# Performance work log

Hardware: AMD Instinct MI355X
Metric: run time of the kernel (lower is better)

## Reference

```python
import jax, jax.numpy as jnp
import numpy as np

N, E, H = 100000, 3200000, 128


def setup_inputs() -> dict:
    key = jax.random.key(0)
    ks = jax.random.split(key, 12)
    s = 1.0 / np.sqrt(H)
    x = jax.random.normal(ks[0], (N, H), dtype=jnp.float32)
    edge_index = jax.random.randint(ks[1], (2, E), 0, N, dtype=jnp.int64)
    # GatedGraphConv weight: [num_layers=1, H, H] -> single [H, H]
    W = jax.random.normal(ks[2], (H, H), dtype=jnp.float32) * s
    # GRUCell (gate order: r, z, n)
    gru_w_ih = jax.random.normal(ks[3], (3 * H, H), dtype=jnp.float32) * s
    gru_w_hh = jax.random.normal(ks[4], (3 * H, H), dtype=jnp.float32) * s
    gru_b_ih = jax.random.normal(ks[5], (3 * H,), dtype=jnp.float32) * s
    gru_b_hh = jax.random.normal(ks[6], (3 * H,), dtype=jnp.float32) * s
    # LSTM layer 0 (gate order: i, f, g, o)
    lstm_w_ih = jax.random.normal(ks[7], (4 * H, H), dtype=jnp.float32) * s
    lstm_w_hh = jax.random.normal(ks[8], (4 * H, H), dtype=jnp.float32) * s
    lstm_b_ih = jax.random.normal(ks[9], (4 * H,), dtype=jnp.float32) * s
    lstm_b_hh = jax.random.normal(ks[10], (4 * H,), dtype=jnp.float32) * s
    return {
        "x": x, "edge_index": edge_index, "W": W,
        "gru_w_ih": gru_w_ih, "gru_w_hh": gru_w_hh,
        "gru_b_ih": gru_b_ih, "gru_b_hh": gru_b_hh,
        "lstm_w_ih": lstm_w_ih, "lstm_w_hh": lstm_w_hh,
        "lstm_b_ih": lstm_b_ih, "lstm_b_hh": lstm_b_hh,
    }


def _forward(x, edge_index, W, gru_w_ih, gru_w_hh, gru_b_ih, gru_b_hh,
             lstm_w_ih, lstm_w_hh, lstm_b_ih, lstm_b_hh):
    n = x.shape[0]
    src, dst = edge_index[0], edge_index[1]
    # GatedGraphConv, num_layers=1, mean aggregation
    m = x @ W                                   # [N, H]
    msg = m[src]                                # [E, H] gather (memory-bound)
    agg_sum = jax.ops.segment_sum(msg, dst, num_segments=n)
    deg = jax.ops.segment_sum(jnp.ones((src.shape[0],), x.dtype), dst, num_segments=n)
    agg = agg_sum / jnp.maximum(deg, 1.0)[:, None]
    # GRUCell(agg, x): gates r, z, n
    gi = agg @ gru_w_ih.T + gru_b_ih
    gh = x @ gru_w_hh.T + gru_b_hh
    i_r, i_z, i_n = jnp.split(gi, 3, axis=-1)
    h_r, h_z, h_n = jnp.split(gh, 3, axis=-1)
    r = jax.nn.sigmoid(i_r + h_r)
    z = jax.nn.sigmoid(i_z + h_z)
    ng = jnp.tanh(i_n + r * h_n)
    h_conv = (1.0 - z) * ng + z * x             # conv output H_tilde
    # 1-layer LSTM over seq_len=1 with zero initial (H, C)
    gates = h_conv @ lstm_w_ih.T + lstm_b_ih + lstm_b_hh  # h0 = 0
    i_g, f_g, g_g, o_g = jnp.split(gates, 4, axis=-1)
    c = jax.nn.sigmoid(i_g) * jnp.tanh(g_g)
    h_lstm = jax.nn.sigmoid(o_g) * jnp.tanh(c)
    return jax.nn.relu(h_lstm)


def reference(x, edge_index, W, gru_w_ih, gru_w_hh, gru_b_ih, gru_b_hh,
              lstm_w_ih, lstm_w_hh, lstm_b_ih, lstm_b_hh):
    return _forward(x, edge_index, W, gru_w_ih, gru_w_hh, gru_b_ih, gru_b_hh,
                    lstm_w_ih, lstm_w_hh, lstm_b_ih, lstm_b_hh)
```

## Files before the change

### kernel.cpp

```cpp
#include <hip/hip_runtime.h>
#include <math.h>

#define HD 128
#define PB 256
#define SCB 4096

typedef __attribute__((ext_vector_type(8))) short short8;
typedef __attribute__((ext_vector_type(4))) float f32x4;

__device__ __forceinline__ float sigf(float v) { return 1.0f / (1.0f + __expf(-v)); }

__device__ __forceinline__ unsigned short f2bf(float f) {
  union { float f; unsigned u; } v; v.f = f;
  unsigned r = (v.u + 0x7fffu + ((v.u >> 16) & 1u)) >> 16;
  return (unsigned short)r;
}
__device__ __forceinline__ float bf2f(unsigned short b) {
  union { unsigned u; float f; } v; v.u = ((unsigned)b) << 16;
  return v.f;
}


__global__ __launch_bounds__(256) void bcount_k(const int* __restrict__ ei,
                                                int* __restrict__ bcnt,
                                                int E, int N, int shift, int NB) {
  __shared__ int h[256];
  const int blk = blockIdx.x, tid = threadIdx.x;
  h[tid] = 0;
  __syncthreads();
  int per = (E + PB - 1) / PB;
  int lo = blk * per;
  int hi = (lo + per < E) ? lo + per : E;
  for (int e = lo + tid; e < hi; e += 256) {
    int d = ei[(size_t)E + e];
    if ((unsigned)d >= (unsigned)N) continue;
    atomicAdd(&h[d >> shift], 1);
  }
  __syncthreads();
  if (tid < NB) bcnt[tid * PB + blk] = h[tid];
}

__global__ __launch_bounds__(256) void scan1_k(const int* __restrict__ a,
                                               int* __restrict__ bsums, int total) {
  __shared__ int ts[256];
  int b = blockIdx.x, tid = threadIdx.x;
  int lo = b * SCB + tid * 16;
  int s = 0;
#pragma unroll
  for (int i = 0; i < 16; ++i) {
    int idx = lo + i;
    if (idx < total) s += a[idx];
  }
  ts[tid] = s;
  __syncthreads();
  for (int off = 128; off > 0; off >>= 1) {
    if (tid < off) ts[tid] += ts[tid + off];
    __syncthreads();
  }
  if (tid == 0) bsums[b] = ts[0];
}

__global__ __launch_bounds__(256) void scan2_k(int* __restrict__ bsums, int nb) {
  __shared__ int ts[256];
  int tid = threadIdx.x;
  int v = (tid < nb) ? bsums[tid] : 0;
  ts[tid] = v;
  __syncthreads();
  for (int off = 1; off < 256; off <<= 1) {
    int u = (tid >= off) ? ts[tid - off] : 0;
    __syncthreads();
    ts[tid] += u;
    __syncthreads();
  }
  if (tid < nb) bsums[tid] = ts[tid] - v;
}

__global__ __launch_bounds__(256) void scan3_k(int* __restrict__ a,
                                               const int* __restrict__ bsums,
                                               int total, int nblk) {
  __shared__ int ts[256];
  int b = blockIdx.x, tid = threadIdx.x;
  int lo = b * SCB + tid * 16;
  int pre[16];
  int s = 0;
#pragma unroll
  for (int i = 0; i < 16; ++i) {
    int idx = lo + i;
    int xv = (idx < total) ? a[idx] : 0;
    pre[i] = s;
    s += xv;
  }
  ts[tid] = s;
  __syncthreads();
  for (int off = 1; off < 256; off <<= 1) {
    int u = (tid >= off) ? ts[tid - off] : 0;
    __syncthreads();
    ts[tid] += u;
    __syncthreads();
  }
  int off0 = ts[tid] - s + bsums[b];
#pragma unroll
  for (int i = 0; i < 16; ++i) {
    int idx = lo + i;
    if (idx < total) a[idx] = off0 + pre[i];
  }
  if (b == nblk - 1 && tid == 255) a[total] = off0 + s;
}

__global__ __launch_bounds__(256) void bpart_k(const int* __restrict__ ei,
                                               const int* __restrict__ bstart,
                                               int2* __restrict__ ebuf,
                                               int E, int N, int shift, int NB) {
  __shared__ int cur[256];
  const int blk = blockIdx.x, tid = threadIdx.x;
  if (tid < NB) cur[tid] = bstart[tid * PB + blk];
  __syncthreads();
  int per = (E + PB - 1) / PB;
  int lo = blk * per;
  int hi = (lo + per < E) ? lo + per : E;
  for (int e = lo + tid; e < hi; e += 256) {
    int s = ei[e];
    int d = ei[(size_t)E + e];
    if ((unsigned)s >= (unsigned)N || (unsigned)d >= (unsigned)N) continue;
    int p = atomicAdd(&cur[d >> shift], 1);
    ebuf[p] = make_int2(s, d);
  }
}

__global__ __launch_bounds__(256) void bfill2_k(const int2* __restrict__ ebuf,
                                                const int* __restrict__ bstart,
                                                int* __restrict__ rowstart,
                                                int* __restrict__ csr,
                                                int N, int shift, int NB) {
  __shared__ int cnt[2048];
  __shared__ int tsum[256];
  const int b = blockIdx.x, tid = threadIdx.x;
  const int d0 = b << shift;
  int dmax = d0 + (1 << shift);
  if (dmax > N) dmax = N;
  const int nd = dmax - d0;
  for (int i = tid; i < nd; i += 256) cnt[i] = 0;
  __syncthreads();
  const int base = bstart[b * PB];
  const int end = bstart[(b + 1) * PB];
  for (int idx = base + tid; idx < end; idx += 256)
    atomicAdd(&cnt[ebuf[idx].y - d0], 1);
  __syncthreads();
  const int C = (nd + 255) / 256;
  int lo = tid * C;
  int hi = (lo + C < nd) ? lo + C : nd;
  int loc[8];
  int s = 0;
  for (int i = lo; i < hi; ++i) {
    loc[i - lo] = cnt[i];
    s += cnt[i];
  }
  tsum[tid] = s;
  __syncthreads();
  for (int off = 1; off < 256; off <<= 1) {
    int u = (tid >= off) ? tsum[tid - off] : 0;
    __syncthreads();
    tsum[tid] += u;
    __syncthreads();
  }
  int run = tsum[tid] - s + base;
  for (int i = lo; i < hi; ++i) {
    rowstart[d0 + i] = run;
    cnt[i] = run;
    run += loc[i - lo];
  }
  if (b == NB - 1 && tid == 255) rowstart[N] = end;
  __syncthreads();
  for (int idx = base + tid; idx < end; idx += 256) {
    int2 sd = ebuf[idx];
    int p = atomicAdd(&cnt[sd.y - d0], 1);
    csr[p] = sd.x;
  }
}


__global__ __launch_bounds__(256) void convx_k(const float* __restrict__ x,
                                               unsigned short* __restrict__ xb, int n4) {
  int t = blockIdx.x * 256 + threadIdx.x;
  if (t >= n4) return;
  float4 v = reinterpret_cast<const float4*>(x)[t];
  ushort4 o;
  o.x = f2bf(v.x); o.y = f2bf(v.y); o.z = f2bf(v.z); o.w = f2bf(v.w);
  reinterpret_cast<ushort4*>(xb)[t] = o;
}

__global__ __launch_bounds__(256) void prepw_k(
    const float* __restrict__ W, const float* __restrict__ gwih,
    const float* __restrict__ gwhh, const float* __restrict__ lwih,
    const float* __restrict__ lbih, const float* __restrict__ lbhh,
    unsigned short* __restrict__ Wt, unsigned short* __restrict__ gwihb,
    unsigned short* __restrict__ gwhhb, unsigned short* __restrict__ lwb,
    float* __restrict__ lbias) {
  int t = blockIdx.x * 256 + threadIdx.x;
  if (t < 16384) {
    int n = t >> 7, k = t & 127;
    Wt[t] = f2bf(W[(size_t)k * 128 + n]);
    return;
  }
  t -= 16384;
  if (t < 49152) { gwihb[t] = f2bf(gwih[t]); return; }
  t -= 49152;
  if (t < 49152) { gwhhb[t] = f2bf(gwhh[t]); return; }
  t -= 49152;
  if (t < 49152) {
    int j = t >> 7, k = t & 127;
    int jm = j < 128 ? j : j + 128;
    lwb[t] = f2bf(lwih[(size_t)jm * 128 + k]);
    return;
  }
  t -= 49152;
  if (t < 384) {
    int jm = t < 128 ? t : t + 128;
    lbias[t] = lbih[jm] + lbhh[jm];
  }
}


__global__ __launch_bounds__(256) void gather_b_k(const int* __restrict__ csr,
                                                  const int* __restrict__ rowstart,
                                                  const unsigned short* __restrict__ xb,
                                                  unsigned short* __restrict__ xaggb, int N) {
  int w = (int)(((long long)blockIdx.x * 256 + threadIdx.x) >> 6);
  if (w >= N) return;
  int lane = threadIdx.x & 63;
  int beg = rowstart[w], end = rowstart[w + 1];
  const unsigned* x1 = reinterpret_cast<const unsigned*>(xb);
  float ax = 0.f, ay = 0.f;
  int j = beg;
  for (; j + 4 <= end; j += 4) {
    int s0 = csr[j], s1 = csr[j + 1], s2 = csr[j + 2], s3 = csr[j + 3];
    unsigned u0 = x1[(size_t)s0 * 64 + lane];
    unsigned u1 = x1[(size_t)s1 * 64 + lane];
    unsigned u2 = x1[(size_t)s2 * 64 + lane];
    unsigned u3 = x1[(size_t)s3 * 64 + lane];
    ax += bf2f((unsigned short)u0) + bf2f((unsigned short)u1) +
          bf2f((unsigned short)u2) + bf2f((unsigned short)u3);
    ay += bf2f((unsigned short)(u0 >> 16)) + bf2f((unsigned short)(u1 >> 16)) +
          bf2f((unsigned short)(u2 >> 16)) + bf2f((unsigned short)(u3 >> 16));
  }
  for (; j < end; ++j) {
    unsigned u = x1[(size_t)csr[j] * 64 + lane];
    ax += bf2f((unsigned short)u);
    ay += bf2f((unsigned short)(u >> 16));
  }
  float scale = 1.0f / fmaxf((float)(end - beg), 1.0f);
  unsigned o = (unsigned)f2bf(ax * scale) | ((unsigned)f2bf(ay * scale) << 16);
  reinterpret_cast<unsigned*>(xaggb)[(size_t)w * 64 + lane] = o;
}

__global__ __launch_bounds__(256) void gemmw_k(const unsigned short* __restrict__ A,
                                               const unsigned short* __restrict__ B,
                                               unsigned short* __restrict__ C, int nrows) {
  __shared__ unsigned short Bs[64][136];
  const int tid = threadIdx.x;
  const int w = tid >> 6, lane = tid & 63;
  const int q = lane >> 4, r = lane & 15;
  const int row0 = blockIdx.y * 64;
  const int col0 = blockIdx.x * 64;

#pragma unroll
  for (int i = 0; i < 4; ++i) {
    int idx = i * 256 + tid;
    int c = idx >> 4, kq = idx & 15;
    uint4 v = *reinterpret_cast<const uint4*>(&B[((size_t)(col0 + c)) * HD + kq * 8]);
    *reinterpret_cast<uint4*>(&Bs[c][kq * 8]) = v;
  }
  __syncthreads();

  int arow = row0 + (w << 4) + r;
  int ar = arow < nrows ? arow : nrows - 1;
  const unsigned short* Ap = A + (size_t)ar * HD + q * 8;

  f32x4 acc[4];
#pragma unroll
  for (int cb = 0; cb < 4; ++cb) acc[cb] = (f32x4)0.f;

#pragma unroll
  for (int ks = 0; ks < 4; ++ks) {
    short8 af = *reinterpret_cast<const short8*>(Ap + ks * 32);
#pragma unroll
    for (int cb = 0; cb < 4; ++cb) {
      short8 bf = *reinterpret_cast<const short8*>(&Bs[cb * 16 + r][ks * 32 + q * 8]);
      acc[cb] = __builtin_amdgcn_mfma_f32_16x16x32_bf16(af, bf, acc[cb], 0, 0, 0);
    }
  }

#pragma unroll
  for (int cb = 0; cb < 4; ++cb) {
    int col = col0 + cb * 16 + r;
#pragma unroll
    for (int reg = 0; reg < 4; ++reg) {
      int row = row0 + (w << 4) + q * 4 + reg;
      if (row < nrows) C[(size_t)row * HD + col] = f2bf(acc[cb][reg]);
    }
  }
}

__global__ __launch_bounds__(256) void gru_fused_k(
    const unsigned short* __restrict__ Acb, const unsigned short* __restrict__ xb,
    const unsigned short* __restrict__ gwihb, const unsigned short* __restrict__ gwhhb,
    const float* __restrict__ gbih, const float* __restrict__ gbhh,
    unsigned short* __restrict__ hconv, int nrows) {
  __shared__ unsigned short Bsm[6][32][136];
  const int tid = threadIdx.x;
  const int w = tid >> 6, lane = tid & 63;
  const int q = lane >> 4, r = lane & 15;
  const int row0 = blockIdx.y * 64;
  const int c0 = blockIdx.x * 32;

#pragma unroll
  for (int it = 0; it < 12; ++it) {
    int idx = it * 256 + tid;
    int p = idx >> 9;
    int rem = idx & 511;
    int col = rem >> 4, kq = rem & 15;
    const unsigned short* src =
        (p < 3) ? gwihb + ((size_t)(p * 128 + c0 + col)) * HD
                : gwhhb + ((size_t)((p - 3) * 128 + c0 + col)) * HD;
    uint4 v = *reinterpret_cast<const uint4*>(src + kq * 8);
    *reinterpret_cast<uint4*>(&Bsm[p][col][kq * 8]) = v;
  }
  __syncthreads();

  int arow = row0 + (w << 4) + r;
  int ar = arow < nrows ? arow : nrows - 1;
  const unsigned short* Aa = Acb + (size_t)ar * HD + q * 8;
  const unsigned short* Ax = xb + (size_t)ar * HD + q * 8;

  f32x4 acc[6][2];
#pragma unroll
  for (int p = 0; p < 6; ++p)
#pragma unroll
    for (int cb = 0; cb < 2; ++cb) acc[p][cb] = (f32x4)0.f;

#pragma unroll
  for (int ks = 0; ks < 4; ++ks) {
    short8 a1 = *reinterpret_cast<const short8*>(Aa + ks * 32);
    short8 a2 = *reinterpret_cast<const short8*>(Ax + ks * 32);
#pragma unroll
    for (int p = 0; p < 6; ++p) {
      short8 af = (p < 3) ? a1 : a2;
#pragma unroll
      for (int cb = 0; cb < 2; ++cb) {
        short8 bf = *reinterpret_cast<const short8*>(&Bsm[p][cb * 16 + r][ks * 32 + q * 8]);
        acc[p][cb] = __builtin_amdgcn_mfma_f32_16x16x32_bf16(af, bf, acc[p][cb], 0, 0, 0);
      }
    }
  }

#pragma unroll
  for (int cb = 0; cb < 2; ++cb) {
    int col = c0 + cb * 16 + r;
    float bir = gbih[col], biz = gbih[col + 128], bin = gbih[col + 256];
    float bhr = gbhh[col], bhz = gbhh[col + 128], bhn = gbhh[col + 256];
#pragma unroll
    for (int reg = 0; reg < 4; ++reg) {
      int row = row0 + (w << 4) + q * 4 + reg;
      if (row < nrows) {
        float ir = acc[0][cb][reg] + bir, iz = acc[1][cb][reg] + biz;
        float inn = acc[2][cb][reg] + bin;
        float hr = acc[3][cb][reg] + bhr, hz = acc[4][cb][reg] + bhz;
        float hn = acc[5][cb][reg] + bhn;
        float rr = sigf(ir + hr), zz = sigf(iz + hz);
        float nn = tanhf(inn + rr * hn);
        float xv = bf2f(xb[(size_t)row * HD + col]);
        hconv[(size_t)row * HD + col] = f2bf((1.f - zz) * nn + zz * xv);
      }
    }
  }
}

__global__ __launch_bounds__(256) void lstm_fused_k(
    const unsigned short* __restrict__ hconv, const unsigned short* __restrict__ lwb,
    const float* __restrict__ lbias, float* __restrict__ out, int nrows) {
  __shared__ unsigned short Bsm[3][64][136];
  const int tid = threadIdx.x;
  const int w = tid >> 6, lane = tid & 63;
  const int q = lane >> 4, r = lane & 15;
  const int row0 = blockIdx.y * 64;
  const int c0 = blockIdx.x * 64;

#pragma unroll
  for (int it = 0; it < 12; ++it) {
    int idx = it * 256 + tid;
    int p = idx >> 10, rem = idx & 1023;
    int col = rem >> 4, kq = rem & 15;
    uint4 v = *reinterpret_cast<const uint4*>(
        lwb + ((size_t)(p * 128 + c0 + col)) * HD + kq * 8);
    *reinterpret_cast<uint4*>(&Bsm[p][col][kq * 8]) = v;
  }
  __syncthreads();

  int arow = row0 + (w << 4) + r;
  int ar = arow < nrows ? arow : nrows - 1;
  const unsigned short* Ap = hconv + (size_t)ar * HD + q * 8;

  f32x4 acc[3][4];
#pragma unroll
  for (int p = 0; p < 3; ++p)
#pragma unroll
    for (int cb = 0; cb < 4; ++cb) acc[p][cb] = (f32x4)0.f;

#pragma unroll
  for (int ks = 0; ks < 4; ++ks) {
    short8 af = *reinterpret_cast<const short8*>(Ap + ks * 32);
#pragma unroll
    for (int p = 0; p < 3; ++p)
#pragma unroll
      for (int cb = 0; cb < 4; ++cb) {
        short8 bf = *reinterpret_cast<const short8*>(&Bsm[p][cb * 16 + r][ks * 32 + q * 8]);
        acc[p][cb] = __builtin_amdgcn_mfma_f32_16x16x32_bf16(af, bf, acc[p][cb], 0, 0, 0);
      }
  }

#pragma unroll
  for (int cb = 0; cb < 4; ++cb) {
    int col = c0 + cb * 16 + r;
    float bi = lbias[col], bg = lbias[col + 128], bo = lbias[col + 256];
#pragma unroll
    for (int reg = 0; reg < 4; ++reg) {
      int row = row0 + (w << 4) + q * 4 + reg;
      if (row < nrows) {
        float ig = acc[0][cb][reg] + bi;
        float gg = acc[1][cb][reg] + bg;
        float og = acc[2][cb][reg] + bo;
        float cc = sigf(ig) * tanhf(gg);
        out[(size_t)row * HD + col] = fmaxf(sigf(og) * tanhf(cc), 0.f);
      }
    }
  }
}


extern "C" void kernel_launch(void* const* d_in, const int* in_sizes, int n_in,
                              void* d_out, int out_size, void* d_ws, size_t ws_size,
                              hipStream_t stream) {
  const float* x = (const float*)d_in[0];
  const int* ei = (const int*)d_in[1];
  const float* W = (const float*)d_in[2];
  const float* gw_ih = (const float*)d_in[3];
  const float* gw_hh = (const float*)d_in[4];
  const float* gb_ih = (const float*)d_in[5];
  const float* gb_hh = (const float*)d_in[6];
  const float* lw_ih = (const float*)d_in[7];
  const float* lb_ih = (const float*)d_in[9];
  const float* lb_hh = (const float*)d_in[10];
  float* out = (float*)d_out;

  const int N = in_sizes[0] / HD;
  const int E = in_sizes[1] / 2;
  const size_t nH = (size_t)N * HD;

  int shift = 9;
  while (((N + (1 << shift) - 1) >> shift) > 256) ++shift;
  const int NB = (N + (1 << shift) - 1) >> shift;

  const size_t N4p = (size_t)((N + 1 + 7) & ~7);
  const size_t E4 = (size_t)((E + 3) & ~3);
  const size_t BC = (size_t)NB * PB + 8;
  const int sc_total = NB * PB;
  const int sc_nblk = (sc_total + SCB - 1) / SCB;

  char* p = (char*)d_ws;
  int* rowstart = (int*)p;  p += 4 * N4p;
  int* bcnt = (int*)p;      p += 4 * BC;
  int* bsums = (int*)p;     p += 4 * 64;
  int* csr = (int*)p;       p += 4 * E4;
  size_t sz_eb = 8 * E4, sz_xb = 2 * nH;
  int2* ebuf = (int2*)p;
  unsigned short* xb = (unsigned short*)p;
  p += (sz_eb > sz_xb ? sz_eb : sz_xb);
  unsigned short* Acb = (unsigned short*)p;    p += 2 * nH;
  unsigned short* hconv = (unsigned short*)p;  p += 2 * nH;
  unsigned short* Wt = (unsigned short*)p;     p += 2 * 16384;
  unsigned short* gwihb = (unsigned short*)p;  p += 2 * 49152;
  unsigned short* gwhhb = (unsigned short*)p;  p += 2 * 49152;
  unsigned short* lwb = (unsigned short*)p;    p += 2 * 49152;
  float* lbias = (float*)p;                    p += 4 * 384;

  unsigned short* xaggb = (unsigned short*)d_out;

  dim3 blk(256);
  unsigned rb = (unsigned)((N + 63) / 64);

  bcount_k<<<PB, blk, 0, stream>>>(ei, bcnt, E, N, shift, NB);
  scan1_k<<<sc_nblk, blk, 0, stream>>>(bcnt, bsums, sc_total);
  scan2_k<<<1, blk, 0, stream>>>(bsums, sc_nblk);
  scan3_k<<<sc_nblk, blk, 0, stream>>>(bcnt, bsums, sc_total, sc_nblk);
  bpart_k<<<PB, blk, 0, stream>>>(ei, bcnt, ebuf, E, N, shift, NB);
  bfill2_k<<<NB, blk, 0, stream>>>(ebuf, bcnt, rowstart, csr, N, shift, NB);

  convx_k<<<(unsigned)((nH / 4 + 255) / 256), blk, 0, stream>>>(x, xb, (int)(nH / 4));
  prepw_k<<<(16384 + 3 * 49152 + 384 + 255) / 256, blk, 0, stream>>>(
      W, gw_ih, gw_hh, lw_ih, lb_ih, lb_hh, Wt, gwihb, gwhhb, lwb, lbias);

  long long gthreads = (long long)N * 64;
  gather_b_k<<<(unsigned)((gthreads + 255) / 256), blk, 0, stream>>>(
      csr, rowstart, xb, xaggb, N);

  gemmw_k<<<dim3(2, rb), blk, 0, stream>>>(xaggb, Wt, Acb, N);

  gru_fused_k<<<dim3(4, rb), blk, 0, stream>>>(
      Acb, xb, gwihb, gwhhb, gb_ih, gb_hh, hconv, N);

  lstm_fused_k<<<dim3(2, rb), blk, 0, stream>>>(hconv, lwb, lbias, out, N);
}
```

Before: 520.8 us.

## Pack edge buffer into 32-bit words and widen gather to 16-byte loads

The bucket-partition buffer now stores each edge as one 32-bit word holding the local destination offset and the source index, instead of an int2. This halves the intermediate traffic in bpart and bfill2. The gather kernel now has each wavefront split into four 16-lane groups, each loading a full 256-byte bf16 row with uint4 loads, so it handles four or eight edges per step and then reduces the groups with shuffles. This gives wider memory transactions and more loads in flight. The packing assumes the source index fits in 32-shift bits. A dead leftover macro is defined and immediately undefined.

```diff
diff --git a/kernel.cpp b/kernel.cpp
--- a/kernel.cpp
+++ b/kernel.cpp
@@ -109,8 +109,9 @@
 
 __global__ __launch_bounds__(256) void bpart_k(const int* __restrict__ ei,
                                                const int* __restrict__ bstart,
-                                               int2* __restrict__ ebuf,
-                                               int E, int N, int shift, int NB) {
+                                               unsigned* __restrict__ ebuf,
+                                               int E, int N, int shift, int NB,
+                                               int sbits) {
   __shared__ int cur[256];
   const int blk = blockIdx.x, tid = threadIdx.x;
   if (tid < NB) cur[tid] = bstart[tid * PB + blk];
@@ -118,20 +119,21 @@
   int per = (E + PB - 1) / PB;
   int lo = blk * per;
   int hi = (lo + per < E) ? lo + per : E;
+  const unsigned dmask = (1u << shift) - 1u;
   for (int e = lo + tid; e < hi; e += 256) {
     int s = ei[e];
     int d = ei[(size_t)E + e];
     if ((unsigned)s >= (unsigned)N || (unsigned)d >= (unsigned)N) continue;
     int p = atomicAdd(&cur[d >> shift], 1);
-    ebuf[p] = make_int2(s, d);
-  }
-}
-
-__global__ __launch_bounds__(256) void bfill2_k(const int2* __restrict__ ebuf,
+    ebuf[p] = (((unsigned)d & dmask) << sbits) | (unsigned)s;
+  }
+}
+
+__global__ __launch_bounds__(256) void bfill2_k(const unsigned* __restrict__ ebuf,
                                                 const int* __restrict__ bstart,
                                                 int* __restrict__ rowstart,
                                                 int* __restrict__ csr,
-                                                int N, int shift, int NB) {
+                                                int N, int shift, int NB, int sbits) {
   __shared__ int cnt[2048];
   __shared__ int tsum[256];
   const int b = blockIdx.x, tid = threadIdx.x;
@@ -139,12 +141,13 @@
   int dmax = d0 + (1 << shift);
   if (dmax > N) dmax = N;
   const int nd = dmax - d0;
+  const unsigned smask = (1u << sbits) - 1u;
   for (int i = tid; i < nd; i += 256) cnt[i] = 0;
   __syncthreads();
   const int base = bstart[b * PB];
   const int end = bstart[(b + 1) * PB];
   for (int idx = base + tid; idx < end; idx += 256)
-    atomicAdd(&cnt[ebuf[idx].y - d0], 1);
+    atomicAdd(&cnt[ebuf[idx] >> sbits], 1);
   __syncthreads();
   const int C = (nd + 255) / 256;
   int lo = tid * C;
@@ -172,9 +175,9 @@
   if (b == NB - 1 && tid == 255) rowstart[N] = end;
   __syncthreads();
   for (int idx = base + tid; idx < end; idx += 256) {
-    int2 sd = ebuf[idx];
-    int p = atomicAdd(&cnt[sd.y - d0], 1);
-    csr[p] = sd.x;
+    unsigned pk = ebuf[idx];
+    int p = atomicAdd(&cnt[pk >> sbits], 1);
+    csr[p] = (int)(pk & smask);
   }
 }
 
@@ -220,37 +223,87 @@
   }
 }
 
-
 __global__ __launch_bounds__(256) void gather_b_k(const int* __restrict__ csr,
                                                   const int* __restrict__ rowstart,
                                                   const unsigned short* __restrict__ xb,
                                                   unsigned short* __restrict__ xaggb, int N) {
   int w = (int)(((long long)blockIdx.x * 256 + threadIdx.x) >> 6);
   if (w >= N) return;
-  int lane = threadIdx.x & 63;
-  int beg = rowstart[w], end = rowstart[w + 1];
-  const unsigned* x1 = reinterpret_cast<const unsigned*>(xb);
-  float ax = 0.f, ay = 0.f;
+  const int lane = threadIdx.x & 63;
+  const int sub = lane >> 4, li = lane & 15;
+  const int beg = rowstart[w], end = rowstart[w + 1];
+  const uint4* x4 = reinterpret_cast<const uint4*>(xb);
+
+  float acc[8] = {0.f, 0.f, 0.f, 0.f, 0.f, 0.f, 0.f, 0.f};
+#define ACC8(v)                                           \
+  {                                                       \
+    acc[0] += bf2f((unsigned short)(v).x);                \
+    acc[1] += bf2f((unsigned short)((v).x >> 16));        \
+    acc[2] += bf2f((unsigned short)(v).y);                \
+    acc[3] += bf2f((unsigned short)((v).y >> 16));        \
+    acc[4] += bf2f((unsigned short)(v).z);                \
+    acc[5] += bf2f((unsigned short)(v).w >> 0 ? (unsigned short)(v).w : (unsigned short)(v).w); \
+    acc[5] += 0.f;                                        \
+  }
+#undef ACC8
+
   int j = beg;
-  for (; j + 4 <= end; j += 4) {
-    int s0 = csr[j], s1 = csr[j + 1], s2 = csr[j + 2], s3 = csr[j + 3];
-    unsigned u0 = x1[(size_t)s0 * 64 + lane];
-    unsigned u1 = x1[(size_t)s1 * 64 + lane];
-    unsigned u2 = x1[(size_t)s2 * 64 + lane];
-    unsigned u3 = x1[(size_t)s3 * 64 + lane];
-    ax += bf2f((unsigned short)u0) + bf2f((unsigned short)u1) +
-          bf2f((unsigned short)u2) + bf2f((unsigned short)u3);
-    ay += bf2f((unsigned short)(u0 >> 16)) + bf2f((unsigned short)(u1 >> 16)) +
-          bf2f((unsigned short)(u2 >> 16)) + bf2f((unsigned short)(u3 >> 16));
-  }
-  for (; j < end; ++j) {
-    unsigned u = x1[(size_t)csr[j] * 64 + lane];
-    ax += bf2f((unsigned short)u);
-    ay += bf2f((unsigned short)(u >> 16));
-  }
-  float scale = 1.0f / fmaxf((float)(end - beg), 1.0f);
-  unsigned o = (unsigned)f2bf(ax * scale) | ((unsigned)f2bf(ay * scale) << 16);
-  reinterpret_cast<unsigned*>(xaggb)[(size_t)w * 64 + lane] = o;
+  for (; j + 8 <= end; j += 8) {
+    int s0 = csr[j + sub];
+    int s1 = csr[j + 4 + sub];
+    uint4 v0 = x4[(size_t)s0 * 16 + li];
+    uint4 v1 = x4[(size_t)s1 * 16 + li];
+    acc[0] += bf2f((unsigned short)v0.x) + bf2f((unsigned short)v1.x);
+    acc[1] += bf2f((unsigned short)(v0.x >> 16)) + bf2f((unsigned short)(v1.x >> 16));
+    acc[2] += bf2f((unsigned short)v0.y) + bf2f((unsigned short)v1.y);
+    acc[3] += bf2f((unsigned short)(v0.y >> 16)) + bf2f((unsigned short)(v1.y >> 16));
+    acc[4] += bf2f((unsigned short)v0.z) + bf2f((unsigned short)v1.z);
+    acc[5] += bf2f((unsigned short)(v0.z >> 16)) + bf2f((unsigned short)(v1.z >> 16));
+    acc[6] += bf2f((unsigned short)v0.w) + bf2f((unsigned short)v1.w);
+    acc[7] += bf2f((unsigned short)(v0.w >> 16)) + bf2f((unsigned short)(v1.w >> 16));
+  }
+  if (j + 4 <= end) {
+    int s0 = csr[j + sub];
+    uint4 v0 = x4[(size_t)s0 * 16 + li];
+    acc[0] += bf2f((unsigned short)v0.x);
+    acc[1] += bf2f((unsigned short)(v0.x >> 16));
+    acc[2] += bf2f((unsigned short)v0.y);
+    acc[3] += bf2f((unsigned short)(v0.y >> 16));
+    acc[4] += bf2f((unsigned short)v0.z);
+    acc[5] += bf2f((unsigned short)(v0.z >> 16));
+    acc[6] += bf2f((unsigned short)v0.w);
+    acc[7] += bf2f((unsigned short)(v0.w >> 16));
+    j += 4;
+  }
+  int rem = end - j;
+  if (sub < rem) {
+    int s0 = csr[j + sub];
+    uint4 v0 = x4[(size_t)s0 * 16 + li];
+    acc[0] += bf2f((unsigned short)v0.x);
+    acc[1] += bf2f((unsigned short)(v0.x >> 16));
+    acc[2] += bf2f((unsigned short)v0.y);
+    acc[3] += bf2f((unsigned short)(v0.y >> 16));
+    acc[4] += bf2f((unsigned short)v0.z);
+    acc[5] += bf2f((unsigned short)(v0.z >> 16));
+    acc[6] += bf2f((unsigned short)v0.w);
+    acc[7] += bf2f((unsigned short)(v0.w >> 16));
+  }
+
+#pragma unroll
+  for (int i = 0; i < 8; ++i) {
+    acc[i] += __shfl_xor(acc[i], 16, 64);
+    acc[i] += __shfl_xor(acc[i], 32, 64);
+  }
+
+  if (lane < 16) {
+    float scale = 1.0f / fmaxf((float)(end - beg), 1.0f);
+    uint4 o;
+    o.x = (unsigned)f2bf(acc[0] * scale) | ((unsigned)f2bf(acc[1] * scale) << 16);
+    o.y = (unsigned)f2bf(acc[2] * scale) | ((unsigned)f2bf(acc[3] * scale) << 16);
+    o.z = (unsigned)f2bf(acc[4] * scale) | ((unsigned)f2bf(acc[5] * scale) << 16);
+    o.w = (unsigned)f2bf(acc[6] * scale) | ((unsigned)f2bf(acc[7] * scale) << 16);
+    reinterpret_cast<uint4*>(xaggb)[(size_t)w * 16 + li] = o;
+  }
 }
 
 __global__ __launch_bounds__(256) void gemmw_k(const unsigned short* __restrict__ A,
@@ -459,6 +512,7 @@
   int shift = 9;
   while (((N + (1 << shift) - 1) >> shift) > 256) ++shift;
   const int NB = (N + (1 << shift) - 1) >> shift;
+  const int sbits = 32 - shift;
 
   const size_t N4p = (size_t)((N + 1 + 7) & ~7);
   const size_t E4 = (size_t)((E + 3) & ~3);
@@ -471,8 +525,8 @@
   int* bcnt = (int*)p;      p += 4 * BC;
   int* bsums = (int*)p;     p += 4 * 64;
   int* csr = (int*)p;       p += 4 * E4;
-  size_t sz_eb = 8 * E4, sz_xb = 2 * nH;
-  int2* ebuf = (int2*)p;
+  size_t sz_eb = 4 * E4, sz_xb = 2 * nH;
+  unsigned* ebuf = (unsigned*)p;
   unsigned short* xb = (unsigned short*)p;
   p += (sz_eb > sz_xb ? sz_eb : sz_xb);
   unsigned short* Acb = (unsigned short*)p;    p += 2 * nH;
@@ -492,8 +546,8 @@
   scan1_k<<<sc_nblk, blk, 0, stream>>>(bcnt, bsums, sc_total);
   scan2_k<<<1, blk, 0, stream>>>(bsums, sc_nblk);
   scan3_k<<<sc_nblk, blk, 0, stream>>>(bcnt, bsums, sc_total, sc_nblk);
-  bpart_k<<<PB, blk, 0, stream>>>(ei, bcnt, ebuf, E, N, shift, NB);
-  bfill2_k<<<NB, blk, 0, stream>>>(ebuf, bcnt, rowstart, csr, N, shift, NB);
+  bpart_k<<<PB, blk, 0, stream>>>(ei, bcnt, ebuf, E, N, shift, NB, sbits);
+  bfill2_k<<<NB, blk, 0, stream>>>(ebuf, bcnt, rowstart, csr, N, shift, NB, sbits);
 
   convx_k<<<(unsigned)((nH / 4 + 255) / 256), blk, 0, stream>>>(x, xb, (int)(nH / 4));
   prepw_k<<<(16384 + 3 * 49152 + 384 + 255) / 256, blk, 0, stream>>>(
```

Result: no change. 511.2 us (-1.8%).
